# Kernel tuning notes

Measured on AMD Instinct MI355X. Metric: run time of the kernel, lower is better.

The kernel has to match this reference:

```python
import jax, jax.numpy as jnp
import numpy as np

DIM = 192
HEADS = 4


def setup_inputs() -> dict:
    key = jax.random.key(0)
    ks = jax.random.split(key, 6)
    b, h, w = 8, 128, 128
    return {
        "x": jax.random.normal(ks[0], (b, DIM, h, w), jnp.float32),
        "svp_fea": jax.random.normal(ks[1], (b, 3, h, w), jnp.float32),
        "qkv_w": jax.random.normal(ks[2], (3 * DIM, DIM), jnp.float32) * 0.02,
        "dw_w": jax.random.normal(ks[3], (3 * DIM, 1, 3, 3), jnp.float32) * 0.02,
        "svp_w": jax.random.normal(ks[4], (3 * HEADS, 3), jnp.float32) * 0.02,
        "proj_w": jax.random.normal(ks[5], (DIM, DIM + 3 * HEADS), jnp.float32) * 0.02,
        "temperature": jnp.ones((HEADS, 1, 1), jnp.float32),
    }


def _l2norm(t):
    # F.normalize(t, dim=-1): divide by max(||t||_2, eps)
    return t / jnp.maximum(jnp.linalg.norm(t, axis=-1, keepdims=True), 1e-12)


def reference(x, svp_fea, qkv_w, dw_w, svp_w, proj_w, temperature):
    b, c, h, w = x.shape
    heads = temperature.shape[0]
    # 1x1 conv (dim -> 3*dim), then 3x3 depthwise conv (groups = 3*dim)
    qkv = jnp.einsum('bchw,oc->bohw', x, qkv_w)
    qkv = jax.lax.conv_general_dilated(
        qkv, dw_w, window_strides=(1, 1), padding=((1, 1), (1, 1)),
        dimension_numbers=('NCHW', 'OIHW', 'NCHW'), feature_group_count=3 * c)
    # 1x1 conv on illumination prior: 3 -> 3*heads
    svp_q = jnp.einsum('bchw,oc->bohw', svp_fea, svp_w)
    q, k, v = jnp.split(qkv, 3, axis=1)
    ch = c // heads
    hw = h * w
    q = _l2norm(q.reshape(b, heads, ch, hw))
    k = _l2norm(k.reshape(b, heads, ch, hw))
    v = v.reshape(b, heads, ch, hw)
    sq = _l2norm(svp_q.reshape(b, heads, 3, hw))
    q = jnp.concatenate([q, sq], axis=2)            # [b, head, ch+3, hw]
    logits = jnp.einsum('bhcn,bhdn->bhcd', q, k) * temperature[None]
    attn = jax.nn.softmax(logits, axis=-1)          # softmax over channel dim d
    out = jnp.einsum('bhcd,bhdn->bhcn', attn, v)    # [b, head, ch+3, hw]
    out = out.reshape(b, heads * (ch + 3), h, w)
    return jnp.einsum('bchw,oc->bohw', out, proj_w)
```

## Files before the change

kernel.cpp:

```cpp
#include <hip/hip_runtime.h>
#include <hip/hip_bf16.h>
#include <math.h>

#define BB   8
#define CCH  192
#define OCN  576
#define HWD  128
#define HWN  16384
#define NH   4
#define CHD  48
#define C51  51
#define GSZ  (C51*48)

typedef __hip_bfloat16 bf16;
typedef __attribute__((ext_vector_type(8))) short short8;
typedef __attribute__((ext_vector_type(4))) float f32x4;

__device__ __forceinline__ float bfbits2f(unsigned int u16) {
  union { unsigned int i; float f; } v; v.i = u16 << 16; return v.f;
}
__device__ __forceinline__ unsigned short f2bfbits(float f) {
  __hip_bfloat16 h = __float2bfloat16(f);
  return *(unsigned short*)&h;
}
__device__ __forceinline__ void stage16(const void* g, void* l) {
  __builtin_amdgcn_global_load_lds(
      (const __attribute__((address_space(1))) void*)g,
      (__attribute__((address_space(3))) void*)l, 16, 0, 0);
}

__global__ __launch_bounds__(256) void k_svp(
    const float* __restrict__ svp_fea, const float* __restrict__ svp_w,
    float* __restrict__ svp_q, float* __restrict__ ssq_svp_p)
{
  __shared__ float lsw[4][12];
  const int b = blockIdx.y;
  const int t = threadIdx.x;
  const int n = blockIdx.x * 256 + t;
  const int wave = t >> 6;
  const float* fb = svp_fea + (size_t)b * 3 * HWN;
  const float f0 = fb[n], f1 = fb[HWN + n], f2 = fb[2 * HWN + n];
  float* ob = svp_q + (size_t)b * 12 * HWN + n;
  #pragma unroll
  for (int r = 0; r < 12; ++r) {
    float o = svp_w[r*3]*f0 + svp_w[r*3+1]*f1 + svp_w[r*3+2]*f2;
    ob[(size_t)r * HWN] = o;
    float v = o * o;
    #pragma unroll
    for (int off = 32; off >= 1; off >>= 1) v += __shfl_down(v, off, 64);
    if ((t & 63) == 0) lsw[wave][r] = v;
  }
  __syncthreads();
  if (t < 12) {
    float s = lsw[0][t] + lsw[1][t] + lsw[2][t] + lsw[3][t];
    ssq_svp_p[((size_t)b * 12 + t) * 64 + blockIdx.x] = s;
  }
}

__global__ __launch_bounds__(256) void k_castw(
    const float* __restrict__ w, unsigned short* __restrict__ wb)
{
  const int i = (blockIdx.x * 256 + threadIdx.x) * 4;
  float4 v = *(const float4*)(w + i);
  union { uint2 u; unsigned short s[4]; } pk;
  pk.s[0] = f2bfbits(v.x); pk.s[1] = f2bfbits(v.y);
  pk.s[2] = f2bfbits(v.z); pk.s[3] = f2bfbits(v.w);
  *(uint2*)(wb + i) = pk.u;
}

__global__ __launch_bounds__(256) void k_gemm(
    const float* __restrict__ x, const unsigned short* __restrict__ wb,
    unsigned short* __restrict__ qkv1)
{
  __shared__ unsigned short Xs[128 * CCH];
  __shared__ unsigned short Wd[2][32 * CCH];
  const int b = blockIdx.y;
  const int n0 = blockIdx.x * 128;
  const int t = threadIdx.x;
  const int lane = t & 63, wave = t >> 6;
  const int wm = wave >> 1, wn = wave & 1;
  const int lq = lane >> 4, lr = lane & 15;

  #pragma unroll
  for (int i = 0; i < 3; ++i) {
    int chunk = wave * 3 + i;
    int d = chunk * 64 + lane;
    int row = d / 24, kg = d % 24;
    int skg = (kg & ~7) | ((kg & 7) ^ (row & 7));
    stage16(wb + (size_t)row * CCH + skg * 8, &Wd[0][0] + chunk * 512);
  }

  const float* xb = x + (size_t)b * CCH * HWN + n0;
  #pragma unroll
  for (int rr = 0; rr < 12; ++rr) {
    int idx = rr * 256 + t;
    int cp = idx >> 5, nq = idx & 31;
    int c0 = cp * 2;
    float4 v0 = *(const float4*)(xb + (size_t)c0 * HWN + nq * 4);
    float4 v1 = *(const float4*)(xb + (size_t)(c0 + 1) * HWN + nq * 4);
    int g = c0 >> 3, co = c0 & 7;
    float a0[4] = {v0.x, v0.y, v0.z, v0.w};
    float a1[4] = {v1.x, v1.y, v1.z, v1.w};
    #pragma unroll
    for (int j = 0; j < 4; ++j) {
      int n = nq * 4 + j;
      int gs = (g & ~7) | ((g & 7) ^ (n & 7) ^ ((n >> 3) & 7));
      unsigned int pk = (unsigned int)f2bfbits(a0[j])
                      | ((unsigned int)f2bfbits(a1[j]) << 16);
      *(unsigned int*)&Xs[n * CCH + gs * 8 + co] = pk;
    }
  }
  __syncthreads();

  short8 bfr[4][6];
  #pragma unroll
  for (int nf = 0; nf < 4; ++nf) {
    int r = wn * 64 + nf * 16 + lr;
    #pragma unroll
    for (int ks = 0; ks < 6; ++ks) {
      int gk = ks * 4 + lq;
      int sg = (gk & ~7) | ((gk & 7) ^ (r & 7) ^ ((r >> 3) & 7));
      bfr[nf][ks] = *(const short8*)&Xs[r * CCH + sg * 8];
    }
  }
  __syncthreads();

  unsigned short* T = &Xs[0];

  for (int mc = 0; mc < 18; ++mc) {
    if (mc + 1 < 18) {
      const unsigned short* wsrc = wb + (size_t)(mc + 1) * 32 * CCH;
      unsigned short* nb = &Wd[(mc + 1) & 1][0];
      #pragma unroll
      for (int i = 0; i < 3; ++i) {
        int chunk = wave * 3 + i;
        int d = chunk * 64 + lane;
        int row = d / 24, kg = d % 24;
        int skg = (kg & ~7) | ((kg & 7) ^ (row & 7));
        stage16(wsrc + (size_t)row * CCH + skg * 8, nb + chunk * 512);
      }
      asm volatile("s_waitcnt vmcnt(3)" ::: "memory");
    } else {
      asm volatile("s_waitcnt vmcnt(0)" ::: "memory");
    }
    __builtin_amdgcn_s_barrier();
    asm volatile("" ::: "memory");

    const unsigned short* wbuf = &Wd[mc & 1][0];
    f32x4 acc[4];
    #pragma unroll
    for (int nf = 0; nf < 4; ++nf) acc[nf] = (f32x4)0.f;

    #pragma unroll
    for (int ks = 0; ks < 6; ++ks) {
      const int gk = ks * 4 + lq;
      int rW = wm * 16 + lr;
      int sg = (gk & ~7) | ((gk & 7) ^ (rW & 7));
      short8 w8 = *(const short8*)&wbuf[rW * CCH + sg * 8];
      #pragma unroll
      for (int nf = 0; nf < 4; ++nf)
        acc[nf] = __builtin_amdgcn_mfma_f32_16x16x32_bf16(
            bfr[nf][ks], w8, acc[nf], 0, 0, 0);
    }

    {
      int m = wm * 16 + lr;
      #pragma unroll
      for (int nf = 0; nf < 4; ++nf) {
        union { unsigned long long u; unsigned short s[4]; } pk;
        #pragma unroll
        for (int r = 0; r < 4; ++r) pk.s[r] = f2bfbits(acc[nf][r]);
        int off = (m * 256 + wn * 128 + nf * 32 + lq * 8) ^ ((m & 15) << 4);
        *(unsigned long long*)((char*)T + off) = pk.u;
      }
    }
    asm volatile("s_waitcnt lgkmcnt(0)" ::: "memory");
    __builtin_amdgcn_s_barrier();
    asm volatile("" ::: "memory");
    #pragma unroll
    for (int i = 0; i < 2; ++i) {
      int p = t + 256 * i;
      int row = p >> 4, seg = p & 15;
      int off = (row * 256 + seg * 16) ^ ((row & 15) << 4);
      uint4 v = *(const uint4*)((const char*)T + off);
      *(uint4*)(qkv1 + ((size_t)b * OCN + mc * 32 + row) * HWN + n0 + seg * 8) = v;
    }
    asm volatile("" ::: "memory");
    __builtin_amdgcn_s_barrier();
  }
}

__global__ __launch_bounds__(256) void k_dw(
    const unsigned short* __restrict__ qkv1, const float* __restrict__ dw_w,
    unsigned short* __restrict__ qkv, float* __restrict__ ssq_qk_p)
{
  __shared__ float lsw[4];
  const int b = blockIdx.z, c = blockIdx.y, slab = blockIdx.x;
  const int t = threadIdx.x;
  const int cg = t & 15, rg = t >> 4;
  const int y0 = slab * 32 + rg * 2;
  const unsigned short* src = qkv1 + ((size_t)b * OCN + c) * HWN;
  float w[9];
  #pragma unroll
  for (int i = 0; i < 9; ++i) w[i] = dw_w[c * 9 + i];

  float rows[4][10];
  #pragma unroll
  for (int j = 0; j < 4; ++j) {
    int gr = y0 - 1 + j;
    uint4 B = make_uint4(0u, 0u, 0u, 0u);
    unsigned int Al = 0; unsigned int Cv = 0;
    if ((unsigned)gr < 128u) {
      const unsigned short* rp = src + (size_t)gr * HWD;
      B = *(const uint4*)(rp + cg * 8);
      if (cg > 0)  Al = *(const unsigned int*)(rp + cg * 8 - 2);
      if (cg < 15) Cv = (unsigned int)rp[cg * 8 + 8];
    }
    rows[j][0] = bfbits2f(Al >> 16);
    unsigned int ub[4] = {B.x, B.y, B.z, B.w};
    #pragma unroll
    for (int q = 0; q < 4; ++q) {
      rows[j][1 + 2*q] = bfbits2f(ub[q] & 0xffffu);
      rows[j][2 + 2*q] = bfbits2f(ub[q] >> 16);
    }
    rows[j][9] = bfbits2f(Cv);
  }

  unsigned short* dst = qkv + ((size_t)b * OCN + c) * HWN;
  float ssq = 0.f;
  #pragma unroll
  for (int e = 0; e < 2; ++e) {
    float acc[8];
    #pragma unroll
    for (int i = 0; i < 8; ++i) acc[i] = 0.f;
    #pragma unroll
    for (int j = 0; j < 3; ++j) {
      const float* vr = rows[e + j];
      #pragma unroll
      for (int i = 0; i < 8; ++i)
        acc[i] += w[j*3]*vr[i] + w[j*3+1]*vr[i+1] + w[j*3+2]*vr[i+2];
    }
    union { uint4 u; unsigned short s[8]; } pk;
    #pragma unroll
    for (int i = 0; i < 8; ++i) pk.s[i] = f2bfbits(acc[i]);
    *(uint4*)(dst + (size_t)(y0 + e) * HWD + cg * 8) = pk.u;
    if (c < 384) {
      #pragma unroll
      for (int i = 0; i < 8; ++i) {
        float rv = bfbits2f(pk.s[i]);
        ssq += rv * rv;
      }
    }
  }
  if (c < 384) {
    #pragma unroll
    for (int off = 32; off >= 1; off >>= 1) ssq += __shfl_down(ssq, off, 64);
    if ((t & 63) == 0) lsw[t >> 6] = ssq;
  }
  __syncthreads();
  if (c < 384 && t == 0)
    ssq_qk_p[(((size_t)b * 384 + c) << 2) | slab] =
        lsw[0] + lsw[1] + lsw[2] + lsw[3];
}

__global__ __launch_bounds__(256) void k_gram(
    const unsigned short* __restrict__ qkv, const float* __restrict__ svp_q,
    float* __restrict__ Gp)
{
  __shared__ float Gs[C51 * 50];
  const int chunk = blockIdx.x, h = blockIdx.y, b = blockIdx.z;
  const int t = threadIdx.x;
  const int lane = t & 63, wave = t >> 6;
  const int lq = lane >> 4, lr = lane & 15;
  const unsigned short* qb = qkv + ((size_t)b*OCN + h*CHD)*HWN;
  const unsigned short* kb = qkv + ((size_t)b*OCN + 192 + h*CHD)*HWN;
  const float* sb = svp_q + ((size_t)b*12 + h*3)*HWN;

  for (int idx = t; idx < C51*50; idx += 256) Gs[idx] = 0.f;

  f32x4 acc[3][3], sacc[3];
  #pragma unroll
  for (int mf = 0; mf < 3; ++mf)
    #pragma unroll
    for (int nf = 0; nf < 3; ++nf) acc[mf][nf] = (f32x4)0.f;
  #pragma unroll
  for (int nf = 0; nf < 3; ++nf) sacc[nf] = (f32x4)0.f;

  const int nbase = chunk * 1024 + wave * 256;
  #pragma unroll 4
  for (int ks = 0; ks < 8; ++ks) {
    const int n = nbase + ks * 32 + lq * 8;
    short8 a[3], bb[3];
    #pragma unroll
    for (int mf = 0; mf < 3; ++mf)
      a[mf] = *(const short8*)&qb[(size_t)(mf*16 + lr)*HWN + n];
    #pragma unroll
    for (int nf = 0; nf < 3; ++nf)
      bb[nf] = *(const short8*)&kb[(size_t)(nf*16 + lr)*HWN + n];
    union { short8 s8; unsigned short us[8]; } sv;
    #pragma unroll
    for (int i = 0; i < 8; ++i) sv.us[i] = 0;
    if (lr < 3) {
      const float* sp = sb + (size_t)lr*HWN + n;
      float4 v0 = *(const float4*)sp, v1 = *(const float4*)(sp + 4);
      sv.us[0] = f2bfbits(v0.x); sv.us[1] = f2bfbits(v0.y);
      sv.us[2] = f2bfbits(v0.z); sv.us[3] = f2bfbits(v0.w);
      sv.us[4] = f2bfbits(v1.x); sv.us[5] = f2bfbits(v1.y);
      sv.us[6] = f2bfbits(v1.z); sv.us[7] = f2bfbits(v1.w);
    }
    #pragma unroll
    for (int mf = 0; mf < 3; ++mf)
      #pragma unroll
      for (int nf = 0; nf < 3; ++nf)
        acc[mf][nf] = __builtin_amdgcn_mfma_f32_16x16x32_bf16(
            a[mf], bb[nf], acc[mf][nf], 0, 0, 0);
    #pragma unroll
    for (int nf = 0; nf < 3; ++nf)
      sacc[nf] = __builtin_amdgcn_mfma_f32_16x16x32_bf16(
          sv.s8, bb[nf], sacc[nf], 0, 0, 0);
  }

  __syncthreads();
  for (int w = 0; w < 4; ++w) {
    if (wave == w) {
      #pragma unroll
      for (int mf = 0; mf < 3; ++mf)
        #pragma unroll
        for (int nf = 0; nf < 3; ++nf)
          #pragma unroll
          for (int r = 0; r < 4; ++r)
            Gs[(mf*16 + lq*4 + r)*50 + nf*16 + lr] += acc[mf][nf][r];
      if (lq == 0) {
        #pragma unroll
        for (int nf = 0; nf < 3; ++nf)
          #pragma unroll
          for (int r = 0; r < 3; ++r)
            Gs[(48 + r)*50 + nf*16 + lr] += sacc[nf][r];
      }
    }
    __syncthreads();
  }
  float* Gout = Gp + ((size_t)((b*NH + h) * 16 + chunk)) * GSZ;
  for (int idx = t; idx < GSZ; idx += 256) {
    int row = idx / 48, col = idx - row * 48;
    Gout[idx] = Gs[row*50 + col];
  }
}

__global__ __launch_bounds__(256) void k_attn_fold(
    const float* __restrict__ Gp, const float* __restrict__ ssq_qk_p,
    const float* __restrict__ ssq_svp_p, const float* __restrict__ temperature,
    const float* __restrict__ proj_w, unsigned short* __restrict__ W2bf)
{
  __shared__ float A[GSZ];
  __shared__ float qinv[C51];
  __shared__ float kinv[48];
  const int h = blockIdx.x, b = blockIdx.y;
  const int t = threadIdx.x;
  const float* Gb = Gp + ((size_t)(b*NH + h) * 16) * GSZ;
  if (t < 48) {
    const float* p = ssq_qk_p + (((size_t)b * 384 + 192 + h*48 + t) << 2);
    kinv[t] = 1.f / fmaxf(sqrtf(p[0] + p[1] + p[2] + p[3]), 1e-12f);
  }
  if (t >= 64 && t < 64 + C51) {
    int c = t - 64;
    float ss;
    if (c < 48) {
      const float* p = ssq_qk_p + (((size_t)b * 384 + h*48 + c) << 2);
      ss = p[0] + p[1] + p[2] + p[3];
    } else {
      const float* p = ssq_svp_p + ((size_t)b * 12 + h*3 + (c - 48)) * 64;
      float s0 = 0.f, s1 = 0.f, s2 = 0.f, s3 = 0.f;
      #pragma unroll
      for (int i = 0; i < 16; ++i) {
        float4 v = *(const float4*)(p + i * 4);
        s0 += v.x; s1 += v.y; s2 += v.z; s3 += v.w;
      }
      ss = (s0 + s1) + (s2 + s3);
    }
    qinv[c] = 1.f / fmaxf(sqrtf(ss), 1e-12f);
  }
  for (int idx = t; idx < GSZ; idx += 256) {
    float s = 0.f;
    #pragma unroll
    for (int c = 0; c < 16; ++c) s += Gb[(size_t)c * GSZ + idx];
    A[idx] = s;
  }
  __syncthreads();
  const float temp = temperature[h];
  if (t < C51) {
    float row[48];
    float m = -1e30f;
    const float qi = qinv[t] * temp;
    #pragma unroll
    for (int d = 0; d < 48; ++d) {
      float l = A[t*48 + d] * qi * kinv[d];
      row[d] = l; m = fmaxf(m, l);
    }
    float s = 0.f;
    #pragma unroll
    for (int d = 0; d < 48; ++d) { row[d] = expf(row[d] - m); s += row[d]; }
    const float inv = 1.f / s;
    #pragma unroll
    for (int d = 0; d < 48; ++d) A[t*48 + d] = row[d] * inv;
  }
  __syncthreads();
  for (int idx = t; idx < 192*48; idx += 256) {
    int o = idx / 48, d = idx - o*48;
    const float* pw = proj_w + o*204 + C51*h;
    float s = 0.f;
    #pragma unroll
    for (int c = 0; c < C51; ++c) s += pw[c] * A[c*48 + d];
    W2bf[((size_t)b*CCH + o)*CCH + h*48 + d] = f2bfbits(s);
  }
}

__global__ __launch_bounds__(256) void k_out(
    const unsigned short* __restrict__ qkv, const unsigned short* __restrict__ w2b,
    float* __restrict__ out)
{
  __shared__ unsigned short Vs[64 * CCH];
  __shared__ unsigned short Wd[2][32 * CCH];
  const int b = blockIdx.y;
  const int n0 = blockIdx.x * 64;
  const int t = threadIdx.x;
  const int lane = t & 63, wave = t >> 6;
  const int wm = wave >> 1, wn = wave & 1;
  const int lq = lane >> 4, lr = lane & 15;

  const unsigned short* w2base = w2b + (size_t)b * CCH * CCH;
  #pragma unroll
  for (int i = 0; i < 3; ++i) {
    int chunk = wave * 3 + i;
    int d = chunk * 64 + lane;
    int row = d / 24, kg = d % 24;
    int skg = (kg & ~7) | ((kg & 7) ^ (row & 7));
    stage16(w2base + (size_t)row * CCH + skg * 8, &Wd[0][0] + chunk * 512);
  }

  const unsigned short* vb = qkv + ((size_t)b * OCN + 384) * HWN + n0;
  #pragma unroll
  for (int rr = 0; rr < 3; ++rr) {
    int idx = rr * 256 + t;
    int cp = idx >> 3, nq = idx & 7;
    int c0 = cp * 2;
    uint4 v0 = *(const uint4*)(vb + (size_t)c0 * HWN + nq * 8);
    uint4 v1 = *(const uint4*)(vb + (size_t)(c0 + 1) * HWN + nq * 8);
    union { uint4 u; unsigned short s[8]; } p0, p1;
    p0.u = v0; p1.u = v1;
    int g = c0 >> 3, co = c0 & 7;
    #pragma unroll
    for (int j = 0; j < 8; ++j) {
      int n = nq * 8 + j;
      int gs = (g & ~7) | ((g & 7) ^ (n & 7) ^ ((n >> 3) & 7));
      unsigned int pk = (unsigned int)p0.s[j] | ((unsigned int)p1.s[j] << 16);
      *(unsigned int*)&Vs[n * CCH + gs * 8 + co] = pk;
    }
  }
  __syncthreads();

  short8 bfr[2][6];
  #pragma unroll
  for (int nf = 0; nf < 2; ++nf) {
    int r = wn * 32 + nf * 16 + lr;
    #pragma unroll
    for (int ks = 0; ks < 6; ++ks) {
      int gk = ks * 4 + lq;
      int sg = (gk & ~7) | ((gk & 7) ^ (r & 7) ^ ((r >> 3) & 7));
      bfr[nf][ks] = *(const short8*)&Vs[r * CCH + sg * 8];
    }
  }

  for (int mc = 0; mc < 6; ++mc) {
    if (mc + 1 < 6) {
      const unsigned short* wsrc = w2base + (size_t)(mc + 1) * 32 * CCH;
      unsigned short* nb = &Wd[(mc + 1) & 1][0];
      #pragma unroll
      for (int i = 0; i < 3; ++i) {
        int chunk = wave * 3 + i;
        int d = chunk * 64 + lane;
        int row = d / 24, kg = d % 24;
        int skg = (kg & ~7) | ((kg & 7) ^ (row & 7));
        stage16(wsrc + (size_t)row * CCH + skg * 8, nb + chunk * 512);
      }
      asm volatile("s_waitcnt vmcnt(3)" ::: "memory");
    } else {
      asm volatile("s_waitcnt vmcnt(0)" ::: "memory");
    }
    __builtin_amdgcn_s_barrier();
    asm volatile("" ::: "memory");

    const unsigned short* wbuf = &Wd[mc & 1][0];
    f32x4 acc0 = (f32x4)0.f, acc1 = (f32x4)0.f;
    #pragma unroll
    for (int ks = 0; ks < 6; ++ks) {
      const int gk = ks * 4 + lq;
      int rW = wm * 16 + lr;
      int sg = (gk & ~7) | ((gk & 7) ^ (rW & 7));
      short8 w8 = *(const short8*)&wbuf[rW * CCH + sg * 8];
      acc0 = __builtin_amdgcn_mfma_f32_16x16x32_bf16(bfr[0][ks], w8, acc0, 0, 0, 0);
      acc1 = __builtin_amdgcn_mfma_f32_16x16x32_bf16(bfr[1][ks], w8, acc1, 0, 0, 0);
    }

    float* ob = out + ((size_t)b * CCH + mc * 32 + wm * 16 + lr) * HWN
                + n0 + wn * 32 + lq * 4;
    *(f32x4*)ob = acc0;
    *(f32x4*)(ob + 16) = acc1;
    asm volatile("" ::: "memory");
    __builtin_amdgcn_s_barrier();
  }
}

extern "C" void kernel_launch(void* const* d_in, const int* in_sizes, int n_in,
                              void* d_out, int out_size, void* d_ws, size_t ws_size,
                              hipStream_t stream)
{
  const float* x       = (const float*)d_in[0];
  const float* svp_fea = (const float*)d_in[1];
  const float* qkv_w   = (const float*)d_in[2];
  const float* dw_w    = (const float*)d_in[3];
  const float* svp_w   = (const float*)d_in[4];
  const float* proj_w  = (const float*)d_in[5];
  const float* temp    = (const float*)d_in[6];
  float* outp = (float*)d_out;

  char* ws = (char*)d_ws;
  const size_t off_qkv1   = 0;
  const size_t off_qkv    = off_qkv1  + (size_t)BB*OCN*HWN*2;
  const size_t off_wb     = off_qkv   + (size_t)BB*OCN*HWN*2;
  const size_t off_svpq   = off_wb    + (size_t)OCN*CCH*2;
  const size_t off_ssqqk  = off_svpq  + (size_t)BB*12*HWN*4;
  const size_t off_ssqsvp = off_ssqqk + (size_t)BB*384*4*4;
  const size_t off_Gp     = off_ssqsvp+ (size_t)BB*12*64*4;
  const size_t off_W2     = off_Gp    + (size_t)BB*NH*16*GSZ*4;

  unsigned short* qkv1  = (unsigned short*)(ws + off_qkv1);
  bf16*  qkv     = (bf16*)(ws + off_qkv);
  unsigned short* wb    = (unsigned short*)(ws + off_wb);
  float* svp_q   = (float*)(ws + off_svpq);
  float* ssq_qk_p  = (float*)(ws + off_ssqqk);
  float* ssq_svp_p = (float*)(ws + off_ssqsvp);
  float* Gp      = (float*)(ws + off_Gp);
  unsigned short* W2bf  = (unsigned short*)(ws + off_W2);

  k_castw    <<<dim3(108),         256, 0, stream>>>(qkv_w, wb);
  k_svp      <<<dim3(64, BB),      256, 0, stream>>>(svp_fea, svp_w, svp_q, ssq_svp_p);
  k_gemm     <<<dim3(128, BB),     256, 0, stream>>>(x, wb, qkv1);
  k_dw       <<<dim3(4, OCN, BB),  256, 0, stream>>>(qkv1, dw_w, (unsigned short*)qkv, ssq_qk_p);
  k_gram     <<<dim3(16, NH, BB),  256, 0, stream>>>((const unsigned short*)qkv, svp_q, Gp);
  k_attn_fold<<<dim3(NH, BB),      256, 0, stream>>>(Gp, ssq_qk_p, ssq_svp_p, temp, proj_w, W2bf);
  k_out      <<<dim3(256, BB),     256, 0, stream>>>((const unsigned short*)qkv, W2bf, outp);
}
```

Baseline: 269.4 us.

## Halve GEMM shared X buffer and stage projection output through LDS

The first GEMM kernel now stages the 128-column X tile in two 64-column phases. Each wave pair loads its B fragments in the phase that matches its half, which halves the Xs shared allocation to raise occupancy. The final projection kernel writes each 32x64 accumulator block into swizzled LDS and then stores full contiguous rows to global memory with 16-byte writes, replacing scattered per-lane stores. This adds barriers and extra LDS traffic in both kernels.

```diff
diff --git a/kernel.cpp b/kernel.cpp
--- a/kernel.cpp
+++ b/kernel.cpp
@@ -72,7 +72,7 @@
     const float* __restrict__ x, const unsigned short* __restrict__ wb,
     unsigned short* __restrict__ qkv1)
 {
-  __shared__ unsigned short Xs[128 * CCH];
+  __shared__ unsigned short Xs[64 * CCH];
   __shared__ unsigned short Wd[2][32 * CCH];
   const int b = blockIdx.y;
   const int n0 = blockIdx.x * 128;
@@ -91,39 +91,44 @@
   }
 
   const float* xb = x + (size_t)b * CCH * HWN + n0;
-  #pragma unroll
-  for (int rr = 0; rr < 12; ++rr) {
-    int idx = rr * 256 + t;
-    int cp = idx >> 5, nq = idx & 31;
-    int c0 = cp * 2;
-    float4 v0 = *(const float4*)(xb + (size_t)c0 * HWN + nq * 4);
-    float4 v1 = *(const float4*)(xb + (size_t)(c0 + 1) * HWN + nq * 4);
-    int g = c0 >> 3, co = c0 & 7;
-    float a0[4] = {v0.x, v0.y, v0.z, v0.w};
-    float a1[4] = {v1.x, v1.y, v1.z, v1.w};
-    #pragma unroll
-    for (int j = 0; j < 4; ++j) {
-      int n = nq * 4 + j;
-      int gs = (g & ~7) | ((g & 7) ^ (n & 7) ^ ((n >> 3) & 7));
-      unsigned int pk = (unsigned int)f2bfbits(a0[j])
-                      | ((unsigned int)f2bfbits(a1[j]) << 16);
-      *(unsigned int*)&Xs[n * CCH + gs * 8 + co] = pk;
-    }
-  }
-  __syncthreads();
-
   short8 bfr[4][6];
-  #pragma unroll
-  for (int nf = 0; nf < 4; ++nf) {
-    int r = wn * 64 + nf * 16 + lr;
-    #pragma unroll
-    for (int ks = 0; ks < 6; ++ks) {
-      int gk = ks * 4 + lq;
-      int sg = (gk & ~7) | ((gk & 7) ^ (r & 7) ^ ((r >> 3) & 7));
-      bfr[nf][ks] = *(const short8*)&Xs[r * CCH + sg * 8];
-    }
-  }
-  __syncthreads();
+  #pragma unroll 1
+  for (int ph = 0; ph < 2; ++ph) {
+    #pragma unroll
+    for (int rr = 0; rr < 6; ++rr) {
+      int idx = rr * 256 + t;
+      int cp = idx >> 4, nq = idx & 15;
+      int c0 = cp * 2;
+      const float* xsrc = xb + (size_t)c0 * HWN + ph * 64 + nq * 4;
+      float4 v0 = *(const float4*)xsrc;
+      float4 v1 = *(const float4*)(xsrc + HWN);
+      int g = c0 >> 3, co = c0 & 7;
+      float a0[4] = {v0.x, v0.y, v0.z, v0.w};
+      float a1[4] = {v1.x, v1.y, v1.z, v1.w};
+      #pragma unroll
+      for (int j = 0; j < 4; ++j) {
+        int n = nq * 4 + j;
+        int gs = (g & ~7) | ((g & 7) ^ (n & 7) ^ ((n >> 3) & 7));
+        unsigned int pk = (unsigned int)f2bfbits(a0[j])
+                        | ((unsigned int)f2bfbits(a1[j]) << 16);
+        *(unsigned int*)&Xs[n * CCH + gs * 8 + co] = pk;
+      }
+    }
+    __syncthreads();
+    if (wn == ph) {
+      #pragma unroll
+      for (int nf = 0; nf < 4; ++nf) {
+        int r = nf * 16 + lr;
+        #pragma unroll
+        for (int ks = 0; ks < 6; ++ks) {
+          int gk = ks * 4 + lq;
+          int sg = (gk & ~7) | ((gk & 7) ^ (r & 7) ^ ((r >> 3) & 7));
+          bfr[nf][ks] = *(const short8*)&Xs[r * CCH + sg * 8];
+        }
+      }
+    }
+    __syncthreads();
+  }
 
   unsigned short* T = &Xs[0];
 
@@ -470,6 +475,9 @@
       bfr[nf][ks] = *(const short8*)&Vs[r * CCH + sg * 8];
     }
   }
+  __syncthreads();
+
+  char* T = (char*)&Vs[0];
 
   for (int mc = 0; mc < 6; ++mc) {
     if (mc + 1 < 6) {
@@ -502,10 +510,24 @@
       acc1 = __builtin_amdgcn_mfma_f32_16x16x32_bf16(bfr[1][ks], w8, acc1, 0, 0, 0);
     }
 
-    float* ob = out + ((size_t)b * CCH + mc * 32 + wm * 16 + lr) * HWN
-                + n0 + wn * 32 + lq * 4;
-    *(f32x4*)ob = acc0;
-    *(f32x4*)(ob + 16) = acc1;
+    {
+      int m = wm * 16 + lr;
+      int off0 = (m * 256 + wn * 128 + lq * 16)      ^ ((m & 15) << 4);
+      int off1 = (m * 256 + wn * 128 + lq * 16 + 64) ^ ((m & 15) << 4);
+      *(f32x4*)(T + off0) = acc0;
+      *(f32x4*)(T + off1) = acc1;
+    }
+    asm volatile("s_waitcnt lgkmcnt(0)" ::: "memory");
+    __builtin_amdgcn_s_barrier();
+    asm volatile("" ::: "memory");
+    #pragma unroll
+    for (int i = 0; i < 2; ++i) {
+      int p = t + 256 * i;
+      int row = p >> 4, seg = p & 15;
+      int off = (row * 256 + seg * 16) ^ ((row & 15) << 4);
+      uint4 v = *(const uint4*)(T + off);
+      *(uint4*)(out + ((size_t)b * CCH + mc * 32 + row) * HWN + n0 + seg * 4) = v;
+    }
     asm volatile("" ::: "memory");
     __builtin_amdgcn_s_barrier();
   }
```

Result: no change. 268.3 us (-0.4%).
